# Kernel tuning notes

Measured on AMD Instinct MI355X. Metric: run time of the kernel, lower is better.

## Reference

```python
import jax, jax.numpy as jnp
import numpy as np

N, LT, LV, D, H = 4, 1024, 1024, 1024, 16
HD = D // H
EPS = 1e-12


def layernorm(x, w, b):
    u = x.mean(-1, keepdims=True)
    s = ((x - u) ** 2).mean(-1, keepdims=True)
    return w * (x - u) / jnp.sqrt(s + EPS) + b


def attention(q_in, k_in, v_in, mask, qw, qb, kw, kb, vw, vb):
    # mask: (N, Lq_or_1, Lk) float in {0,1}; torch Linear is x @ W.T + b
    def heads(x, w, b):
        y = x @ w.T + b
        return y.reshape(y.shape[0], y.shape[1], H, HD).transpose(0, 2, 1, 3)  # (N,H,L,hd)
    q, k, v = heads(q_in, qw, qb), heads(k_in, kw, kb), heads(v_in, vw, vb)
    scores = jnp.einsum('bhqd,bhkd->bhqk', q, k) / np.sqrt(HD).astype(np.float32)
    scores = scores + (1.0 - mask[:, None]) * (-10000.0)
    probs = jax.nn.softmax(scores, axis=-1)  # dropout is identity in eval
    ctx = jnp.einsum('bhqk,bhkd->bhqd', probs, v)
    return ctx.transpose(0, 2, 1, 3).reshape(q_in.shape[0], q_in.shape[1], D)


def setup_inputs() -> dict:
    key = jax.random.key(0)
    ks = jax.random.split(key, 16)
    inp = {
        'dec_hidden_states': jax.random.normal(ks[0], (N, LT, D), jnp.float32),
        'enc_outputs': jax.random.normal(ks[1], (N, LV, D), jnp.float32),
        'dec_mask': jnp.ones((N, LT), jnp.float32),
        'enc_mask': jnp.ones((N, LV), jnp.float32),
    }
    wnames = ['sa_qw', 'sa_kw', 'sa_vw', 'ca_qw', 'ca_kw', 'ca_vw', 'out_w']
    for i, n in enumerate(wnames):
        inp[n] = jax.random.normal(ks[2 + i], (D, D), jnp.float32) * 0.02
    for n in ['sa_qb', 'sa_kb', 'sa_vb', 'ca_qb', 'ca_kb', 'ca_vb', 'out_b', 'n1_b', 'n2_b', 'out_ln_b']:
        inp[n] = jnp.zeros((D,), jnp.float32)
    for n in ['n1_w', 'n2_w', 'out_ln_w']:
        inp[n] = jnp.ones((D,), jnp.float32)
    return inp


def reference(dec_hidden_states, enc_outputs, dec_mask, enc_mask,
              sa_qw, sa_qb, sa_kw, sa_kb, sa_vw, sa_vb, n1_w, n1_b,
              ca_qw, ca_qb, ca_kw, ca_kb, ca_vw, ca_vb, n2_w, n2_b,
              out_w, out_b, out_ln_w, out_ln_b):
    Lt = dec_mask.shape[1]
    # diagonal_mask=True: causal tril combined with padding mask
    self_mask = dec_mask[:, None, :] * jnp.tril(jnp.ones((Lt, Lt), dec_mask.dtype))  # (N,Lt,Lt)
    a = attention(dec_hidden_states, dec_hidden_states, dec_hidden_states, self_mask,
                  sa_qw, sa_qb, sa_kw, sa_kb, sa_vw, sa_vb)
    a = layernorm(a + dec_hidden_states, n1_w, n1_b)
    c = attention(a, enc_outputs, enc_outputs, enc_mask[:, None, :],
                  ca_qw, ca_qb, ca_kw, ca_kb, ca_vw, ca_vb)
    c = layernorm(a + c, n2_w, n2_b)
    # BertOutput called as output(x, x): dense, residual, LN (dropout = identity)
    h = c @ out_w.T + out_b
    return layernorm(h + c, out_ln_w, out_ln_b)
```

## Files before the change

### kernel.cpp

```cpp
#include <hip/hip_runtime.h>
#include <cstdint>
#include <cstddef>

typedef __bf16 bf16x8 __attribute__((ext_vector_type(8)));
typedef float  floatx4 __attribute__((ext_vector_type(4)));
typedef unsigned short ushortx8 __attribute__((ext_vector_type(8)));
typedef unsigned short ushortx4 __attribute__((ext_vector_type(4)));

#define MFMA16(a, b, c) __builtin_amdgcn_mfma_f32_16x16x32_bf16((a), (b), (c), 0, 0, 0)

__device__ inline unsigned short f2bf(float f) {
    unsigned int u = __float_as_uint(f);
    unsigned int r = (u + 0x7fffu + ((u >> 16) & 1u)) >> 16;
    return (unsigned short)r;
}

struct Src2 { const float* p[2]; };
__global__ __launch_bounds__(256) void k_x2_to_bf16(Src2 s2, unsigned short* __restrict__ dst) {
    int i = blockIdx.x * 256 + threadIdx.x;
    const float* src = s2.p[i >> 19];
    int off = i & 524287;
    const float4* s = (const float4*)src + (size_t)off * 2;
    float4 x0 = s[0], x1 = s[1];
    ushortx8 o;
    o[0] = f2bf(x0.x); o[1] = f2bf(x0.y); o[2] = f2bf(x0.z); o[3] = f2bf(x0.w);
    o[4] = f2bf(x1.x); o[5] = f2bf(x1.y); o[6] = f2bf(x1.z); o[7] = f2bf(x1.w);
    *((ushortx8*)dst + i) = o;
}
struct Src7 { const float* p[7]; };
__global__ __launch_bounds__(256) void k_w7_to_bf16(Src7 s7, unsigned short* __restrict__ dst) {
    int i = blockIdx.x * 256 + threadIdx.x;
    const float* src = s7.p[i >> 17];
    int off = i & 131071;
    const float4* s = (const float4*)src + (size_t)off * 2;
    float4 x0 = s[0], x1 = s[1];
    ushortx8 o;
    o[0] = f2bf(x0.x); o[1] = f2bf(x0.y); o[2] = f2bf(x0.z); o[3] = f2bf(x0.w);
    o[4] = f2bf(x1.x); o[5] = f2bf(x1.y); o[6] = f2bf(x1.z); o[7] = f2bf(x1.w);
    *((ushortx8*)dst + i) = o;
}

template <int MODE>
__global__ __launch_bounds__(256) void k_gemm_bias(const unsigned short* __restrict__ A,
                                                   const unsigned short* __restrict__ A2,
                                                   const unsigned short* __restrict__ W,
                                                   const float* __restrict__ bias0,
                                                   const float* __restrict__ bias1,
                                                   const float* __restrict__ bias2,
                                                   void* __restrict__ d0,
                                                   void* __restrict__ d1,
                                                   void* __restrict__ d2,
                                                   int K) {
    __shared__ __align__(16) unsigned short As[128 * 64];
    __shared__ __align__(16) unsigned short Bs[128 * 64];
    const int tid = threadIdx.x;
    const int wave = tid >> 6, lane = tid & 63;
    const int quad = lane >> 4, l15 = lane & 15;
    const int wm = wave >> 1, wn = wave & 1;

    constexpr int NT = (MODE == 3) ? 8 : 24;
    int fid = blockIdx.y * 32 + blockIdx.x;
    int xcd = fid & 7, idx = fid >> 3;
    const int m0 = (xcd * 4 + idx / NT) * 128;
    const int n0 = (idx % NT) * 128;
    const int sect_blk = n0 >> 10;

    const unsigned short* Ause = (MODE == 4 && sect_blk != 0) ? A2 : A;

    const size_t rowbytes = (size_t)K * 2;
    const int idx0 = tid, idx1 = 256 + tid;
    const char* pA0 = (const char*)Ause + (size_t)(m0 + (idx0 >> 2)) * rowbytes + ((idx0 & 3) << 4);
    const char* pA1 = (const char*)Ause + (size_t)(m0 + (idx1 >> 2)) * rowbytes + ((idx1 & 3) << 4);
    const char* pB0 = (const char*)W + (size_t)(n0 + (idx0 >> 2)) * rowbytes + ((idx0 & 3) << 4);
    const char* pB1 = (const char*)W + (size_t)(n0 + (idx1 >> 2)) * rowbytes + ((idx1 & 3) << 4);

    int4 a0a = *(const int4*)pA0, a0b = *(const int4*)(pA0 + 64);
    int4 a1a = *(const int4*)pA1, a1b = *(const int4*)(pA1 + 64);
    int4 b0a = *(const int4*)pB0, b0b = *(const int4*)(pB0 + 64);
    int4 b1a = *(const int4*)pB1, b1b = *(const int4*)(pB1 + 64);

    floatx4 acc[4][4] = {};

    const int KT = K >> 6;
    for (int kt = 0; kt < KT; ++kt) {
        __syncthreads();
        ((int4*)As)[idx0] = a0a; ((int4*)As)[idx1] = a1a;
        ((int4*)As)[512 + idx0] = a0b; ((int4*)As)[512 + idx1] = a1b;
        ((int4*)Bs)[idx0] = b0a; ((int4*)Bs)[idx1] = b1a;
        ((int4*)Bs)[512 + idx0] = b0b; ((int4*)Bs)[512 + idx1] = b1b;
        __syncthreads();
        if (kt + 1 < KT) {
            pA0 += 128; pA1 += 128; pB0 += 128; pB1 += 128;
            a0a = *(const int4*)pA0; a0b = *(const int4*)(pA0 + 64);
            a1a = *(const int4*)pA1; a1b = *(const int4*)(pA1 + 64);
            b0a = *(const int4*)pB0; b0b = *(const int4*)(pB0 + 64);
            b1a = *(const int4*)pB1; b1b = *(const int4*)(pB1 + 64);
        }
        const char* Asb = (const char*)As;
        const char* Bsb = (const char*)Bs;
#pragma unroll
        for (int half = 0; half < 2; ++half) {
            const int hb = half * 8192;
            bf16x8 af[4], bfr[4];
#pragma unroll
            for (int r = 0; r < 4; ++r)
                af[r] = *(const bf16x8*)(Asb + hb + ((wm * 64 + r * 16 + l15) * 64 + quad * 16));
#pragma unroll
            for (int c = 0; c < 4; ++c)
                bfr[c] = *(const bf16x8*)(Bsb + hb + ((wn * 64 + c * 16 + l15) * 64 + quad * 16));
#pragma unroll
            for (int r = 0; r < 4; ++r)
#pragma unroll
                for (int c = 0; c < 4; ++c)
                    acc[r][c] = MFMA16(af[r], bfr[c], acc[r][c]);
        }
    }

#pragma unroll
    for (int c = 0; c < 4; ++c) {
        int col = n0 + wn * 64 + c * 16 + l15;
        int sect = col >> 10, cc = col & 1023;
        float bv;
        if (MODE == 3) bv = bias0[col];
        else bv = (sect == 0 ? bias0 : (sect == 1 ? bias1 : bias2))[cc];
        int h = cc >> 6, d = cc & 63;
#pragma unroll
        for (int r = 0; r < 4; ++r) {
            int mrow = m0 + wm * 64 + r * 16 + quad * 4;
#pragma unroll
            for (int i = 0; i < 4; ++i) {
                float v = acc[r][c][i] + bv;
                int row = mrow + i;
                if (MODE == 3) {
                    ((float*)d0)[(size_t)row * 1024 + col] = v;
                } else {
                    int b = row >> 10, l = row & 1023;
                    unsigned short* base = (unsigned short*)(sect == 0 ? d0 : (sect == 1 ? d1 : d2));
                    bool isV = (sect == 2);
                    size_t off;
                    if (isV) {
                        int kk = l & 31;
                        int kperm = ((kk & 15) << 1) | (kk >> 4);
                        off = (size_t)(b * 16 + h) * 65536 + (size_t)(l >> 5) * 2048 + d * 32 + kperm;
                    } else {
                        off = ((size_t)(b * 16 + h) * 1024 + l) * 64 + d;
                    }
                    base[off] = f2bf(v);
                }
            }
        }
    }
}

__global__ __launch_bounds__(256, 2) void k_flash_attn(const unsigned short* __restrict__ Qp,
                                                       const unsigned short* __restrict__ Kp,
                                                       const unsigned short* __restrict__ Vp,
                                                       const float* __restrict__ mask,
                                                       float* __restrict__ ctx,
                                                       int causal) {
    const int L = 1024, D = 1024;
    const float SC = 0.18033688011112042f;
    int f = blockIdx.x;
    int g = f >> 6;
    int bh = (f & 7) + (g << 3);
    int qt = ((f >> 3) + g) & 7;
    int h = bh & 15, b = bh >> 4;
    int tid = threadIdx.x;
    int wave = tid >> 6, lane = tid & 63, quad = lane >> 4, l15 = lane & 15;
    int qbase = qt * 128 + wave * 32;

    __shared__ __align__(16) unsigned short Ks[4096];
    __shared__ __align__(16) unsigned short Vs[5120];
    __shared__ float penf[1024];
    __shared__ __align__(16) unsigned short Plds[4 * 1280];

    {
        float4 mv = ((const float4*)(mask + b * L))[tid];
        float4 pv;
        pv.x = (1.0f - mv.x) * -14426.950408889634f;
        pv.y = (1.0f - mv.y) * -14426.950408889634f;
        pv.z = (1.0f - mv.z) * -14426.950408889634f;
        pv.w = (1.0f - mv.w) * -14426.950408889634f;
        ((float4*)penf)[tid] = pv;
    }

    const unsigned short* Qh = Qp + ((size_t)(b * 16 + h) * 1024 + qbase) * 64;
    bf16x8 qf[2][2];
#pragma unroll
    for (int qh = 0; qh < 2; ++qh) {
        qf[qh][0] = *(const bf16x8*)(Qh + (qh * 16 + l15) * 64 + quad * 8);
        qf[qh][1] = *(const bf16x8*)(Qh + (qh * 16 + l15) * 64 + 32 + quad * 8);
    }

    const char* Kh = (const char*)(Kp + (size_t)(b * 16 + h) * 65536);
    const char* Vh = (const char*)(Vp + (size_t)(b * 16 + h) * 65536);

    int ktiles = causal ? (2 * qt + 2) : 16;

    char* Ksb = (char*)Ks;
    char* Vsb = (char*)Vs;
    int krow = tid >> 3, kblk = tid & 7;
    int kd0 = krow * 128 + ((kblk ^ (krow & 7)) << 4);
    int kd1 = kd0 + 32 * 128;
    int vd0 = (tid >> 2) * 80 + ((tid & 3) << 4);
    int vd1 = vd0 + 5120;

    int karA[4], karB[4];
#pragma unroll
    for (int r = 0; r < 4; ++r) {
        int row = r * 16 + l15;
        karA[r] = row * 128 + ((quad ^ (l15 & 7)) << 4);
        karB[r] = row * 128 + (((quad | 4) ^ (l15 & 7)) << 4);
    }
    int var_[8];
#pragma unroll
    for (int s = 0; s < 2; ++s)
#pragma unroll
        for (int fi = 0; fi < 4; ++fi)
            var_[s * 4 + fi] = s * 5120 + (fi * 16 + l15) * 80 + (quad << 4);

    floatx4 O[2][4] = {};
    float lsum[2][4] = {};
    unsigned short* pw = &Plds[wave * 1280];
    unsigned int* pw32 = (unsigned int*)pw;

    int4 ka0 = *(const int4*)(Kh + tid * 16);
    int4 ka1 = *(const int4*)(Kh + 4096 + tid * 16);
    int4 va0 = *(const int4*)(Vh + tid * 16);
    int4 va1 = *(const int4*)(Vh + 4096 + tid * 16);

    for (int kt = 0; kt < ktiles; ++kt) {
        *(int4*)(Ksb + kd0) = ka0;
        *(int4*)(Ksb + kd1) = ka1;
        *(int4*)(Vsb + vd0) = va0;
        *(int4*)(Vsb + vd1) = va1;
        __syncthreads();
        if (kt + 1 < ktiles) {
            const char* Kg = Kh + (size_t)(kt + 1) * 8192;
            const char* Vg = Vh + (size_t)(kt + 1) * 8192;
            ka0 = *(const int4*)(Kg + tid * 16);
            ka1 = *(const int4*)(Kg + 4096 + tid * 16);
            va0 = *(const int4*)(Vg + tid * 16);
            va1 = *(const int4*)(Vg + 4096 + tid * 16);
        }
        int k0 = kt * 64;

        if (!(causal && k0 > qbase + 31)) {
            bf16x8 kA[4], kB[4];
#pragma unroll
            for (int r = 0; r < 4; ++r) {
                kA[r] = *(const bf16x8*)(Ksb + karA[r]);
                kB[r] = *(const bf16x8*)(Ksb + karB[r]);
            }
            bf16x8 vv[8];
#pragma unroll
            for (int s = 0; s < 8; ++s) vv[s] = *(const bf16x8*)(Vsb + var_[s]);
            float pr0 = penf[k0 + l15];
            float pr1 = penf[k0 + 16 + l15];
            float pr2 = penf[k0 + 32 + l15];
            float pr3 = penf[k0 + 48 + l15];

#pragma unroll
            for (int qh = 0; qh < 2; ++qh) {
                int qlo = qbase + qh * 16;
                if (causal && k0 > qlo + 15) continue;
                bool boundary = causal && (k0 + 63 > qlo);

                floatx4 S0 = {}, S1 = {}, S2 = {}, S3 = {};
                S0 = MFMA16(qf[qh][0], kA[0], S0); S0 = MFMA16(qf[qh][1], kB[0], S0);
                S1 = MFMA16(qf[qh][0], kA[1], S1); S1 = MFMA16(qf[qh][1], kB[1], S1);
                S2 = MFMA16(qf[qh][0], kA[2], S2); S2 = MFMA16(qf[qh][1], kB[2], S2);
                S3 = MFMA16(qf[qh][0], kA[3], S3); S3 = MFMA16(qf[qh][1], kB[3], S3);

                int qrow = qlo + quad * 4;
#pragma unroll
                for (int i = 0; i < 4; ++i) {
                    float x0 = fmaf(S0[i], SC, pr0);
                    float x1 = fmaf(S1[i], SC, pr1);
                    float x2 = fmaf(S2[i], SC, pr2);
                    float x3 = fmaf(S3[i], SC, pr3);
                    if (boundary) {
                        int q = qrow + i;
                        x0 = ((k0 + l15) <= q) ? x0 : -50000.0f;
                        x1 = ((k0 + 16 + l15) <= q) ? x1 : -50000.0f;
                        x2 = ((k0 + 32 + l15) <= q) ? x2 : -50000.0f;
                        x3 = ((k0 + 48 + l15) <= q) ? x3 : -50000.0f;
                    }
                    float p0 = __builtin_amdgcn_exp2f(x0);
                    float p1 = __builtin_amdgcn_exp2f(x1);
                    float p2 = __builtin_amdgcn_exp2f(x2);
                    float p3 = __builtin_amdgcn_exp2f(x3);
                    lsum[qh][i] += (p0 + p1) + (p2 + p3);
                    unsigned r0 = __float_as_uint(p0) + 0x8000u;
                    unsigned r1 = __float_as_uint(p1) + 0x8000u;
                    unsigned r2 = __float_as_uint(p2) + 0x8000u;
                    unsigned r3 = __float_as_uint(p3) + 0x8000u;
                    unsigned plo = __builtin_amdgcn_perm(r1, r0, 0x07060302u);
                    unsigned phi = __builtin_amdgcn_perm(r3, r2, 0x07060302u);
                    int ro = (quad * 4 + i) * 20;
                    pw32[ro + l15] = plo;
                    pw32[320 + ro + l15] = phi;
                }
                bf16x8 pa_lo = *(const bf16x8*)(pw + l15 * 40 + quad * 8);
                bf16x8 pa_hi = *(const bf16x8*)(pw + 640 + l15 * 40 + quad * 8);
                O[qh][0] = MFMA16(pa_lo, vv[0], O[qh][0]);
                O[qh][1] = MFMA16(pa_lo, vv[1], O[qh][1]);
                O[qh][2] = MFMA16(pa_lo, vv[2], O[qh][2]);
                O[qh][3] = MFMA16(pa_lo, vv[3], O[qh][3]);
                O[qh][0] = MFMA16(pa_hi, vv[4], O[qh][0]);
                O[qh][1] = MFMA16(pa_hi, vv[5], O[qh][1]);
                O[qh][2] = MFMA16(pa_hi, vv[6], O[qh][2]);
                O[qh][3] = MFMA16(pa_hi, vv[7], O[qh][3]);
            }
        }
        __syncthreads();
    }

#pragma unroll
    for (int qh = 0; qh < 2; ++qh)
#pragma unroll
        for (int i = 0; i < 4; ++i) {
            float l = lsum[qh][i];
            l += __shfl_xor(l, 1);
            l += __shfl_xor(l, 2);
            l += __shfl_xor(l, 4);
            l += __shfl_xor(l, 8);
            float inv = 1.0f / l;
            int q = qbase + qh * 16 + quad * 4 + i;
            float* op = ctx + ((size_t)(b * L + q)) * D + h * 64;
#pragma unroll
            for (int fi = 0; fi < 4; ++fi) op[fi * 16 + l15] = O[qh][fi][i] * inv;
        }
}

__global__ __launch_bounds__(256) void k_add_ln(const float* __restrict__ X,
                                                const float* __restrict__ Y,
                                                const float* __restrict__ w,
                                                const float* __restrict__ bvec,
                                                float* __restrict__ outf,
                                                unsigned short* __restrict__ outbf) {
    int row = blockIdx.x;
    int tid = threadIdx.x;
    float4 x = *((const float4*)(X + (size_t)row * 1024) + tid);
    float4 y = *((const float4*)(Y + (size_t)row * 1024) + tid);
    float v0 = x.x + y.x, v1 = x.y + y.y, v2 = x.z + y.z, v3 = x.w + y.w;
    float s = v0 + v1 + v2 + v3;
    float s2 = v0 * v0 + v1 * v1 + v2 * v2 + v3 * v3;
#pragma unroll
    for (int off = 32; off > 0; off >>= 1) {
        s += __shfl_xor(s, off);
        s2 += __shfl_xor(s2, off);
    }
    __shared__ float red[8];
    int wave = tid >> 6, lane = tid & 63;
    if (lane == 0) { red[wave] = s; red[4 + wave] = s2; }
    __syncthreads();
    s = red[0] + red[1] + red[2] + red[3];
    s2 = red[4] + red[5] + red[6] + red[7];
    float u = s * (1.0f / 1024.0f);
    float var = s2 * (1.0f / 1024.0f) - u * u;
    float r = 1.0f / sqrtf(fmaxf(var, 0.0f) + 1e-12f);
    float4 wv = *((const float4*)w + tid);
    float4 bv = *((const float4*)bvec + tid);
    float o0 = wv.x * (v0 - u) * r + bv.x;
    float o1 = wv.y * (v1 - u) * r + bv.y;
    float o2 = wv.z * (v2 - u) * r + bv.z;
    float o3 = wv.w * (v3 - u) * r + bv.w;
    float4 o = {o0, o1, o2, o3};
    *((float4*)(outf + (size_t)row * 1024) + tid) = o;
    if (outbf) {
        ushortx4 ob;
        ob[0] = f2bf(o0); ob[1] = f2bf(o1); ob[2] = f2bf(o2); ob[3] = f2bf(o3);
        *((ushortx4*)outbf + (size_t)row * 256 + tid) = ob;
    }
}

extern "C" void kernel_launch(void* const* d_in, const int* in_sizes, int n_in,
                              void* d_out, int out_size, void* d_ws, size_t ws_size,
                              hipStream_t stream) {
    (void)in_sizes; (void)n_in; (void)out_size; (void)ws_size;
    const float* dec = (const float*)d_in[0];
    const float* enc = (const float*)d_in[1];
    const float* dec_mask = (const float*)d_in[2];
    const float* enc_mask = (const float*)d_in[3];
    const float* b_saq = (const float*)d_in[11];
    const float* b_sak = (const float*)d_in[12];
    const float* b_sav = (const float*)d_in[13];
    const float* b_caq = (const float*)d_in[14];
    const float* b_cak = (const float*)d_in[15];
    const float* b_cav = (const float*)d_in[16];
    const float* b_out = (const float*)d_in[17];
    const float* n1_b = (const float*)d_in[18];
    const float* n2_b = (const float*)d_in[19];
    const float* oln_b = (const float*)d_in[20];
    const float* n1_w = (const float*)d_in[21];
    const float* n2_w = (const float*)d_in[22];
    const float* oln_w = (const float*)d_in[23];

    char* ws = (char*)d_ws;
    const size_t MB2 = 2097152;
    const size_t ACT_BF = 8388608;
    const size_t ACT_F32 = 16777216;
    unsigned short* Wbf[7];
    for (int i = 0; i < 7; ++i) Wbf[i] = (unsigned short*)(ws + i * MB2);
    size_t off = 7 * MB2;
    unsigned short* Xbf = (unsigned short*)(ws + off); off += ACT_BF;
    unsigned short* Ebf = (unsigned short*)(ws + off); off += ACT_BF;
    unsigned short* Abf = (unsigned short*)(ws + off); off += ACT_BF;
    unsigned short* Cbf = (unsigned short*)(ws + off); off += ACT_BF;
    unsigned short* Qp = (unsigned short*)(ws + off); off += ACT_BF;
    unsigned short* Kp = (unsigned short*)(ws + off); off += ACT_BF;
    unsigned short* Vp = (unsigned short*)(ws + off); off += ACT_BF;
    float* ctx = (float*)(ws + off); off += ACT_F32;
    float* a_f32 = (float*)(ws + off); off += ACT_F32;
    float* c_f32 = (float*)(ws + off); off += ACT_F32;
    float* h_f32 = ctx;
    float* outp = (float*)d_out;

    dim3 blk(256);
    dim3 attn_grid(512);

    Src2 s2; s2.p[0] = dec; s2.p[1] = enc;
    k_x2_to_bf16<<<dim3(4096), blk, 0, stream>>>(s2, Xbf);
    Src7 s7;
    for (int i = 0; i < 7; ++i) s7.p[i] = (const float*)d_in[4 + i];
    k_w7_to_bf16<<<dim3(3584), blk, 0, stream>>>(s7, Wbf[0]);

    k_gemm_bias<0><<<dim3(32, 24), blk, 0, stream>>>(Xbf, Xbf, Wbf[0], b_saq, b_sak, b_sav,
                                                     Qp, Kp, Vp, 1024);
    k_flash_attn<<<attn_grid, blk, 0, stream>>>(Qp, Kp, Vp, dec_mask, ctx, 1);
    k_add_ln<<<dim3(4096), blk, 0, stream>>>(ctx, dec, n1_w, n1_b, a_f32, Abf);

    k_gemm_bias<4><<<dim3(32, 24), blk, 0, stream>>>(Abf, Ebf, Wbf[3], b_caq, b_cak, b_cav,
                                                     Qp, Kp, Vp, 1024);
    k_flash_attn<<<attn_grid, blk, 0, stream>>>(Qp, Kp, Vp, enc_mask, ctx, 0);
    k_add_ln<<<dim3(4096), blk, 0, stream>>>(a_f32, ctx, n2_w, n2_b, c_f32, Cbf);

    k_gemm_bias<3><<<dim3(32, 8), blk, 0, stream>>>(Cbf, Cbf, Wbf[6], b_out, b_out, b_out,
                                                    h_f32, nullptr, nullptr, 1024);
    k_add_ln<<<dim3(4096), blk, 0, stream>>>(h_f32, c_f32, oln_w, oln_b, outp, (unsigned short*)nullptr);
}
```

Measured before the change: 336.3 us.

## Halve attention query tile to 64 rows and double grid with higher occupancy

The flash-attention kernel now processes 64 query rows per block (16 per wave) instead of 128, launching 1024 blocks instead of 512, with launch bounds raised to 4 blocks per CU. The block-to-tile mapping is reworked so causal work stays spread across blocks, and the causal per-wave skip logic is simplified. This aims to improve parallelism, occupancy and causal load balance. The cost is that each K/V tile loaded into shared memory now serves half as many query rows, so global and LDS traffic per unit of compute roughly doubles.

```diff
diff --git a/kernel.cpp b/kernel.cpp
--- a/kernel.cpp
+++ b/kernel.cpp
@@ -152,7 +152,7 @@
     }
 }
 
-__global__ __launch_bounds__(256, 2) void k_flash_attn(const unsigned short* __restrict__ Qp,
+__global__ __launch_bounds__(256, 4) void k_flash_attn(const unsigned short* __restrict__ Qp,
                                                        const unsigned short* __restrict__ Kp,
                                                        const unsigned short* __restrict__ Vp,
                                                        const float* __restrict__ mask,
@@ -161,13 +161,14 @@
     const int L = 1024, D = 1024;
     const float SC = 0.18033688011112042f;
     int f = blockIdx.x;
-    int g = f >> 6;
+    int g = f >> 7;
+    int q = (f >> 3) & 15;
     int bh = (f & 7) + (g << 3);
-    int qt = ((f >> 3) + g) & 7;
+    int qt = (q + 2 * g) & 15;
     int h = bh & 15, b = bh >> 4;
     int tid = threadIdx.x;
     int wave = tid >> 6, lane = tid & 63, quad = lane >> 4, l15 = lane & 15;
-    int qbase = qt * 128 + wave * 32;
+    int qbase = qt * 64 + wave * 16;
 
     __shared__ __align__(16) unsigned short Ks[4096];
     __shared__ __align__(16) unsigned short Vs[5120];
@@ -185,17 +186,13 @@
     }
 
     const unsigned short* Qh = Qp + ((size_t)(b * 16 + h) * 1024 + qbase) * 64;
-    bf16x8 qf[2][2];
-#pragma unroll
-    for (int qh = 0; qh < 2; ++qh) {
-        qf[qh][0] = *(const bf16x8*)(Qh + (qh * 16 + l15) * 64 + quad * 8);
-        qf[qh][1] = *(const bf16x8*)(Qh + (qh * 16 + l15) * 64 + 32 + quad * 8);
-    }
+    bf16x8 qf0 = *(const bf16x8*)(Qh + l15 * 64 + quad * 8);
+    bf16x8 qf1 = *(const bf16x8*)(Qh + l15 * 64 + 32 + quad * 8);
 
     const char* Kh = (const char*)(Kp + (size_t)(b * 16 + h) * 65536);
     const char* Vh = (const char*)(Vp + (size_t)(b * 16 + h) * 65536);
 
-    int ktiles = causal ? (2 * qt + 2) : 16;
+    int ktiles = causal ? (qt + 1) : 16;
 
     char* Ksb = (char*)Ks;
     char* Vsb = (char*)Vs;
@@ -219,8 +216,8 @@
         for (int fi = 0; fi < 4; ++fi)
             var_[s * 4 + fi] = s * 5120 + (fi * 16 + l15) * 80 + (quad << 4);
 
-    floatx4 O[2][4] = {};
-    float lsum[2][4] = {};
+    floatx4 O[4] = {};
+    float lsum[4] = {};
     unsigned short* pw = &Plds[wave * 1280];
     unsigned int* pw32 = (unsigned int*)pw;
 
@@ -245,92 +242,83 @@
         }
         int k0 = kt * 64;
 
-        if (!(causal && k0 > qbase + 31)) {
-            bf16x8 kA[4], kB[4];
-#pragma unroll
-            for (int r = 0; r < 4; ++r) {
-                kA[r] = *(const bf16x8*)(Ksb + karA[r]);
-                kB[r] = *(const bf16x8*)(Ksb + karB[r]);
+        bf16x8 kA[4], kB[4];
+#pragma unroll
+        for (int r = 0; r < 4; ++r) {
+            kA[r] = *(const bf16x8*)(Ksb + karA[r]);
+            kB[r] = *(const bf16x8*)(Ksb + karB[r]);
+        }
+        bf16x8 vv[8];
+#pragma unroll
+        for (int s = 0; s < 8; ++s) vv[s] = *(const bf16x8*)(Vsb + var_[s]);
+        float pr0 = penf[k0 + l15];
+        float pr1 = penf[k0 + 16 + l15];
+        float pr2 = penf[k0 + 32 + l15];
+        float pr3 = penf[k0 + 48 + l15];
+
+        bool boundary = causal && (k0 + 63 > qbase);
+
+        floatx4 S0 = {}, S1 = {}, S2 = {}, S3 = {};
+        S0 = MFMA16(qf0, kA[0], S0); S0 = MFMA16(qf1, kB[0], S0);
+        S1 = MFMA16(qf0, kA[1], S1); S1 = MFMA16(qf1, kB[1], S1);
+        S2 = MFMA16(qf0, kA[2], S2); S2 = MFMA16(qf1, kB[2], S2);
+        S3 = MFMA16(qf0, kA[3], S3); S3 = MFMA16(qf1, kB[3], S3);
+
+        int qrow = qbase + quad * 4;
+#pragma unroll
+        for (int i = 0; i < 4; ++i) {
+            float x0 = fmaf(S0[i], SC, pr0);
+            float x1 = fmaf(S1[i], SC, pr1);
+            float x2 = fmaf(S2[i], SC, pr2);
+            float x3 = fmaf(S3[i], SC, pr3);
+            if (boundary) {
+                int qq = qrow + i;
+                x0 = ((k0 + l15) <= qq) ? x0 : -50000.0f;
+                x1 = ((k0 + 16 + l15) <= qq) ? x1 : -50000.0f;
+                x2 = ((k0 + 32 + l15) <= qq) ? x2 : -50000.0f;
+                x3 = ((k0 + 48 + l15) <= qq) ? x3 : -50000.0f;
             }
-            bf16x8 vv[8];
-#pragma unroll
-            for (int s = 0; s < 8; ++s) vv[s] = *(const bf16x8*)(Vsb + var_[s]);
-            float pr0 = penf[k0 + l15];
-            float pr1 = penf[k0 + 16 + l15];
-            float pr2 = penf[k0 + 32 + l15];
-            float pr3 = penf[k0 + 48 + l15];
-
-#pragma unroll
-            for (int qh = 0; qh < 2; ++qh) {
-                int qlo = qbase + qh * 16;
-                if (causal && k0 > qlo + 15) continue;
-                bool boundary = causal && (k0 + 63 > qlo);
-
-                floatx4 S0 = {}, S1 = {}, S2 = {}, S3 = {};
-                S0 = MFMA16(qf[qh][0], kA[0], S0); S0 = MFMA16(qf[qh][1], kB[0], S0);
-                S1 = MFMA16(qf[qh][0], kA[1], S1); S1 = MFMA16(qf[qh][1], kB[1], S1);
-                S2 = MFMA16(qf[qh][0], kA[2], S2); S2 = MFMA16(qf[qh][1], kB[2], S2);
-                S3 = MFMA16(qf[qh][0], kA[3], S3); S3 = MFMA16(qf[qh][1], kB[3], S3);
-
-                int qrow = qlo + quad * 4;
-#pragma unroll
-                for (int i = 0; i < 4; ++i) {
-                    float x0 = fmaf(S0[i], SC, pr0);
-                    float x1 = fmaf(S1[i], SC, pr1);
-                    float x2 = fmaf(S2[i], SC, pr2);
-                    float x3 = fmaf(S3[i], SC, pr3);
-                    if (boundary) {
-                        int q = qrow + i;
-                        x0 = ((k0 + l15) <= q) ? x0 : -50000.0f;
-                        x1 = ((k0 + 16 + l15) <= q) ? x1 : -50000.0f;
-                        x2 = ((k0 + 32 + l15) <= q) ? x2 : -50000.0f;
-                        x3 = ((k0 + 48 + l15) <= q) ? x3 : -50000.0f;
-                    }
-                    float p0 = __builtin_amdgcn_exp2f(x0);
-                    float p1 = __builtin_amdgcn_exp2f(x1);
-                    float p2 = __builtin_amdgcn_exp2f(x2);
-                    float p3 = __builtin_amdgcn_exp2f(x3);
-                    lsum[qh][i] += (p0 + p1) + (p2 + p3);
-                    unsigned r0 = __float_as_uint(p0) + 0x8000u;
-                    unsigned r1 = __float_as_uint(p1) + 0x8000u;
-                    unsigned r2 = __float_as_uint(p2) + 0x8000u;
-                    unsigned r3 = __float_as_uint(p3) + 0x8000u;
-                    unsigned plo = __builtin_amdgcn_perm(r1, r0, 0x07060302u);
-                    unsigned phi = __builtin_amdgcn_perm(r3, r2, 0x07060302u);
-                    int ro = (quad * 4 + i) * 20;
-                    pw32[ro + l15] = plo;
-                    pw32[320 + ro + l15] = phi;
-                }
-                bf16x8 pa_lo = *(const bf16x8*)(pw + l15 * 40 + quad * 8);
-                bf16x8 pa_hi = *(const bf16x8*)(pw + 640 + l15 * 40 + quad * 8);
-                O[qh][0] = MFMA16(pa_lo, vv[0], O[qh][0]);
-                O[qh][1] = MFMA16(pa_lo, vv[1], O[qh][1]);
-                O[qh][2] = MFMA16(pa_lo, vv[2], O[qh][2]);
-                O[qh][3] = MFMA16(pa_lo, vv[3], O[qh][3]);
-                O[qh][0] = MFMA16(pa_hi, vv[4], O[qh][0]);
-                O[qh][1] = MFMA16(pa_hi, vv[5], O[qh][1]);
-                O[qh][2] = MFMA16(pa_hi, vv[6], O[qh][2]);
-                O[qh][3] = MFMA16(pa_hi, vv[7], O[qh][3]);
-            }
-        }
+            float p0 = __builtin_amdgcn_exp2f(x0);
+            float p1 = __builtin_amdgcn_exp2f(x1);
+            float p2 = __builtin_amdgcn_exp2f(x2);
+            float p3 = __builtin_amdgcn_exp2f(x3);
+            lsum[i] += (p0 + p1) + (p2 + p3);
+            unsigned r0 = __float_as_uint(p0) + 0x8000u;
+            unsigned r1 = __float_as_uint(p1) + 0x8000u;
+            unsigned r2 = __float_as_uint(p2) + 0x8000u;
+            unsigned r3 = __float_as_uint(p3) + 0x8000u;
+            unsigned plo = __builtin_amdgcn_perm(r1, r0, 0x07060302u);
+            unsigned phi = __builtin_amdgcn_perm(r3, r2, 0x07060302u);
+            int ro = (quad * 4 + i) * 20;
+            pw32[ro + l15] = plo;
+            pw32[320 + ro + l15] = phi;
+        }
+        bf16x8 pa_lo = *(const bf16x8*)(pw + l15 * 40 + quad * 8);
+        bf16x8 pa_hi = *(const bf16x8*)(pw + 640 + l15 * 40 + quad * 8);
+        O[0] = MFMA16(pa_lo, vv[0], O[0]);
+        O[1] = MFMA16(pa_lo, vv[1], O[1]);
+        O[2] = MFMA16(pa_lo, vv[2], O[2]);
+        O[3] = MFMA16(pa_lo, vv[3], O[3]);
+        O[0] = MFMA16(pa_hi, vv[4], O[0]);
+        O[1] = MFMA16(pa_hi, vv[5], O[1]);
+        O[2] = MFMA16(pa_hi, vv[6], O[2]);
+        O[3] = MFMA16(pa_hi, vv[7], O[3]);
         __syncthreads();
     }
 
 #pragma unroll
-    for (int qh = 0; qh < 2; ++qh)
-#pragma unroll
-        for (int i = 0; i < 4; ++i) {
-            float l = lsum[qh][i];
-            l += __shfl_xor(l, 1);
-            l += __shfl_xor(l, 2);
-            l += __shfl_xor(l, 4);
-            l += __shfl_xor(l, 8);
-            float inv = 1.0f / l;
-            int q = qbase + qh * 16 + quad * 4 + i;
-            float* op = ctx + ((size_t)(b * L + q)) * D + h * 64;
-#pragma unroll
-            for (int fi = 0; fi < 4; ++fi) op[fi * 16 + l15] = O[qh][fi][i] * inv;
-        }
+    for (int i = 0; i < 4; ++i) {
+        float l = lsum[i];
+        l += __shfl_xor(l, 1);
+        l += __shfl_xor(l, 2);
+        l += __shfl_xor(l, 4);
+        l += __shfl_xor(l, 8);
+        float inv = 1.0f / l;
+        int qi = qbase + quad * 4 + i;
+        float* op = ctx + ((size_t)(b * L + qi)) * D + h * 64;
+#pragma unroll
+        for (int fi = 0; fi < 4; ++fi) op[fi * 16 + l15] = O[fi][i] * inv;
+    }
 }
 
 __global__ __launch_bounds__(256) void k_add_ln(const float* __restrict__ X,
@@ -418,7 +406,7 @@
     float* outp = (float*)d_out;
 
     dim3 blk(256);
-    dim3 attn_grid(512);
+    dim3 attn_grid(1024);
 
     Src2 s2; s2.p[0] = dec; s2.p[1] = enc;
     k_x2_to_bf16<<<dim3(4096), blk, 0, stream>>>(s2, Xbf);
```

Result: no change. 331.8 us (-1.3%).
